# Optimization experiments

Hardware: AMD Instinct MI355X
Metric: run time of the kernel (lower is better)

## Reference

```python
import jax, jax.numpy as jnp
import numpy as np

Z_DIM = 3
H = 128
N_BLOCKS = 4
N = 30000
E = 180000
T = 2


def _mlp2(x, W1, b1, W2, b2):
    return jnp.maximum(x @ W1 + b1, 0.0) @ W2 + b2


def _stats(x, eps=1e-8):
    # batch mean/std as accumulated by the running-stat Normalizer (buffers -> no grad)
    m = x.mean(0)
    v = jnp.maximum((x * x).mean(0) - m * m, 0.0)
    s = jnp.maximum(jnp.sqrt(v), eps)
    return jax.lax.stop_gradient(m), jax.lax.stop_gradient(s)


def setup_inputs() -> dict:
    key = jax.random.key(0)
    ks = jax.random.split(key, 32)

    def w(k, shape, fan_in):
        return jax.random.normal(k, shape, jnp.float32) / np.sqrt(fan_in).astype(np.float32)

    inp = {}
    inp["z"] = jax.random.normal(ks[0], (T, N, Z_DIM), jnp.float32)
    inp["z_target"] = jax.random.normal(ks[1], (N, Z_DIM), jnp.float32)
    inp["pos"] = jax.random.uniform(ks[2], (N, 2), jnp.float32)
    # encoder node MLP: z_dim -> H -> H
    inp["enc_node_W1"] = w(ks[3], (Z_DIM, H), Z_DIM)
    inp["enc_node_b1"] = jnp.zeros((H,), jnp.float32)
    inp["enc_node_W2"] = w(ks[4], (H, H), H)
    inp["enc_node_b2"] = jnp.zeros((H,), jnp.float32)
    # encoder edge MLP: edge_dim(3) -> H -> H
    inp["enc_edge_W1"] = w(ks[5], (3, H), 3)
    inp["enc_edge_b1"] = jnp.zeros((H,), jnp.float32)
    inp["enc_edge_W2"] = w(ks[6], (H, H), H)
    inp["enc_edge_b2"] = jnp.zeros((H,), jnp.float32)
    # decoder MLP: H -> H -> z_dim
    inp["dec_W1"] = w(ks[7], (H, H), H)
    inp["dec_b1"] = jnp.zeros((H,), jnp.float32)
    inp["dec_W2"] = w(ks[8], (H, Z_DIM), H)
    inp["dec_b2"] = jnp.zeros((Z_DIM,), jnp.float32)
    # GraphNetBlocks, stacked over n_blocks
    inp["blk_edge_W1"] = w(ks[9], (N_BLOCKS, 3 * H, H), 3 * H)
    inp["blk_edge_b1"] = jnp.zeros((N_BLOCKS, H), jnp.float32)
    inp["blk_edge_W2"] = w(ks[10], (N_BLOCKS, H, H), H)
    inp["blk_edge_b2"] = jnp.zeros((N_BLOCKS, H), jnp.float32)
    inp["blk_node_W1"] = w(ks[11], (N_BLOCKS, 2 * H, H), 2 * H)
    inp["blk_node_b1"] = jnp.zeros((N_BLOCKS, H), jnp.float32)
    inp["blk_node_W2"] = w(ks[12], (N_BLOCKS, H, H), H)
    inp["blk_node_b2"] = jnp.zeros((N_BLOCKS, H), jnp.float32)
    # bidirectional mesh edges (triangles_to_edges output)
    inp["senders"] = jax.random.randint(ks[13], (E,), 0, N, jnp.int64)
    inp["receivers"] = jax.random.randint(ks[14], (E,), 0, N, jnp.int64)
    return inp


def reference(z, z_target, pos,
              enc_node_W1, enc_node_b1, enc_node_W2, enc_node_b2,
              enc_edge_W1, enc_edge_b1, enc_edge_W2, enc_edge_b2,
              dec_W1, dec_b1, dec_W2, dec_b2,
              blk_edge_W1, blk_edge_b1, blk_edge_W2, blk_edge_b2,
              blk_node_W1, blk_node_b1, blk_node_W2, blk_node_b2,
              senders, receivers):
    zl = z[-1]                                   # [N, z_dim]
    n_nodes = zl.shape[0]

    # --- build_graph ---
    rel = pos[senders] - pos[receivers]          # [E, 2]
    ef_raw = jnp.concatenate([rel, jnp.linalg.norm(rel, axis=1, keepdims=True)], axis=1)  # [E, 3]
    em, es = _stats(ef_raw)
    ef = _mlp2((ef_raw - em) / es, enc_edge_W1, enc_edge_b1, enc_edge_W2, enc_edge_b2)    # [E, H]
    nm, ns = _stats(zl)
    nf = _mlp2((zl - nm) / ns, enc_node_W1, enc_node_b1, enc_node_W2, enc_node_b2)        # [N, H]

    # --- message passing blocks ---
    def block(carry, p):
        nf, ef = carry
        eW1, eb1, eW2, eb2, nW1, nb1, nW2, nb2 = p
        e_in = jnp.concatenate([ef, nf[senders], nf[receivers]], axis=1)   # [E, 3H]
        ef = _mlp2(e_in, eW1, eb1, eW2, eb2) + ef
        agg = jax.ops.segment_sum(ef, receivers, num_segments=n_nodes)    # [N, H]
        n_in = jnp.concatenate([nf, agg], axis=1)                          # [N, 2H]
        nf = _mlp2(n_in, nW1, nb1, nW2, nb2) + nf
        return (nf, ef), None

    (nf, ef), _ = jax.lax.scan(block, (nf, ef),
                               (blk_edge_W1, blk_edge_b1, blk_edge_W2, blk_edge_b2,
                                blk_node_W1, blk_node_b1, blk_node_W2, blk_node_b2))

    # --- decode + loss ---
    output = _mlp2(nf, dec_W1, dec_b1, dec_W2, dec_b2)                     # [N, z_dim]
    target = z_target - zl
    om, os = _stats(target)
    target_normalized = (target - om) / os
    loss = jnp.mean((target_normalized - output) ** 2)

    z_update = jax.lax.stop_gradient(output) * os + om                     # Normalizer.inverse(detach)
    z_pred = zl + z_update
    rmse = jnp.mean(jnp.sqrt(jnp.mean((z_pred - z_target) ** 2, axis=0)))
    return z_pred, loss, rmse
```

## Files before the change

kernel.cpp:

```cpp
#include <hip/hip_runtime.h>
#include <hip/hip_bf16.h>
#include <math.h>

#define HDIM 128
#define TPB 256

typedef __attribute__((ext_vector_type(8))) short bf16x8;
typedef __attribute__((ext_vector_type(4))) float f32x4;

static inline int ceil_div(int a, int b){ return (a + b - 1) / b; }

__device__ __forceinline__ float wave_sum(float v){
#pragma unroll
  for (int o = 32; o > 0; o >>= 1) v += __shfl_down(v, o, 64);
  return v;
}

__device__ __forceinline__ short f2bf(float f){
  __hip_bfloat16 h = __float2bfloat16(f);
  return *reinterpret_cast<short*>(&h);
}
__device__ __forceinline__ float bfb2f(short s){
  unsigned int u = ((unsigned int)(unsigned short)s) << 16;
  return __builtin_bit_cast(float, u);
}

__device__ __forceinline__ void gl_lds16(const short* g, short* l){
  __builtin_amdgcn_global_load_lds(
      (const __attribute__((address_space(1))) void*)g,
      (__attribute__((address_space(3))) void*)l, 16, 0, 0);
}

__global__ void csr_hist(const int* __restrict__ rcv, int* __restrict__ deg, int E){
  int e = blockIdx.x * blockDim.x + threadIdx.x;
  if (e < E) atomicAdd(&deg[rcv[e]], 1);
}

__global__ void csr_scan(const int* __restrict__ deg, int* __restrict__ row_start,
                         int N, int E){
  __shared__ int part[1024];
  int t = threadIdx.x;
  int chunk = (N + 1023) / 1024;
  int lo = t * chunk, hi = min(lo + chunk, N);
  int s = 0;
  for (int i = lo; i < hi; i++) s += deg[i];
  part[t] = s;
  __syncthreads();
  for (int off = 1; off < 1024; off <<= 1){
    int v = (t >= off) ? part[t - off] : 0;
    __syncthreads();
    part[t] += v;
    __syncthreads();
  }
  int base = (t == 0) ? 0 : part[t - 1];
  for (int i = lo; i < hi; i++){
    row_start[i] = base;
    base += deg[i];
  }
  if (t == 1023) row_start[N] = E;
}

__global__ void edge_prep(const float* __restrict__ pos,
                          const int* __restrict__ snd,
                          const int* __restrict__ rcv,
                          int* __restrict__ cursor,
                          int* __restrict__ psnd,
                          int* __restrict__ prcv,
                          float* __restrict__ ef_raw,
                          float* __restrict__ epart, int E){
  __shared__ float red[4][6];
  int tid = threadIdx.x, w = tid >> 6, l = tid & 63;
  int e = blockIdx.x * blockDim.x + tid;
  float s[6] = {0.f,0.f,0.f,0.f,0.f,0.f};
  if (e < E){
    int si = snd[e], ri = rcv[e];
    int p = atomicAdd(&cursor[ri], 1);
    psnd[p] = si;
    prcv[p] = ri;
    float rx = pos[2*si]   - pos[2*ri];
    float ry = pos[2*si+1] - pos[2*ri+1];
    float nm = sqrtf(rx*rx + ry*ry);
    ef_raw[3*p]   = rx;
    ef_raw[3*p+1] = ry;
    ef_raw[3*p+2] = nm;
    s[0] = rx; s[1] = ry; s[2] = nm;
    s[3] = rx*rx; s[4] = ry*ry; s[5] = nm*nm;
  }
#pragma unroll
  for (int k = 0; k < 6; k++) s[k] = wave_sum(s[k]);
  if (l == 0)
#pragma unroll
    for (int k = 0; k < 6; k++) red[w][k] = s[k];
  __syncthreads();
  if (tid < 6)
    epart[(size_t)blockIdx.x * 6 + tid] =
      red[0][tid] + red[1][tid] + red[2][tid] + red[3][tid];
}

__global__ void node_stats(const float* __restrict__ zl,
                           const float* __restrict__ z_target,
                           float* __restrict__ npart, int N){
  __shared__ float red[4][12];
  int tid = threadIdx.x, w = tid >> 6, l = tid & 63;
  int n = blockIdx.x * blockDim.x + tid;
  float s[12];
#pragma unroll
  for (int i = 0; i < 12; i++) s[i] = 0.f;
  if (n < N){
#pragma unroll
    for (int d = 0; d < 3; d++){
      float z = zl[3*n+d];
      float t = z_target[3*n+d] - z;
      s[d]   = z;  s[3+d] = z*z;
      s[6+d] = t;  s[9+d] = t*t;
    }
  }
#pragma unroll
  for (int i = 0; i < 12; i++) s[i] = wave_sum(s[i]);
  if (l == 0)
#pragma unroll
    for (int i = 0; i < 12; i++) red[w][i] = s[i];
  __syncthreads();
  if (tid < 12)
    npart[(size_t)blockIdx.x * 12 + tid] =
      red[0][tid] + red[1][tid] + red[2][tid] + red[3][tid];
}

__global__ void reduce_stats(const float* __restrict__ ep, int ne,
                             const float* __restrict__ np_, int nn,
                             float* __restrict__ raw){
  __shared__ float red[4];
  int tid = threadIdx.x, w = tid >> 6, l = tid & 63;
  for (int j = 0; j < 6; j++){
    float s = 0.f;
    for (int b = tid; b < ne; b += 256) s += ep[(size_t)b * 6 + j];
    s = wave_sum(s);
    if (l == 0) red[w] = s;
    __syncthreads();
    if (tid == 0) raw[j] = red[0] + red[1] + red[2] + red[3];
    __syncthreads();
  }
  for (int j = 0; j < 12; j++){
    float s = 0.f;
    for (int b = tid; b < nn; b += 256) s += np_[(size_t)b * 12 + j];
    s = wave_sum(s);
    if (l == 0) red[w] = s;
    __syncthreads();
    if (tid == 0) raw[6 + j] = red[0] + red[1] + red[2] + red[3];
    __syncthreads();
  }
}

__global__ void finalize_stats(const float* __restrict__ raw,
                               float* __restrict__ fin, int E, int N){
#pragma unroll
  for (int d = 0; d < 3; d++){
    float cE = (float)E, cN = (float)N;
    float m, v;
    m = raw[0+d] / cE; v = fmaxf(raw[3+d]/cE - m*m, 0.f);
    fin[0+d] = m;  fin[3+d]  = fmaxf(sqrtf(v), 1e-8f);
    m = raw[6+d] / cN; v = fmaxf(raw[9+d]/cN - m*m, 0.f);
    fin[6+d] = m;  fin[9+d]  = fmaxf(sqrtf(v), 1e-8f);
    m = raw[12+d] / cN; v = fmaxf(raw[15+d]/cN - m*m, 0.f);
    fin[12+d] = m; fin[15+d] = fmaxf(sqrtf(v), 1e-8f);
  }
}

__global__ void pack_weights(const float* __restrict__ encEW2,
                             const float* __restrict__ encNW2,
                             const float* __restrict__ decW1,
                             const float* __restrict__ beW1,
                             const float* __restrict__ beW2,
                             const float* __restrict__ bnW1,
                             const float* __restrict__ bnW2,
                             __hip_bfloat16* __restrict__ wp){
  int y = blockIdx.y;
  const float* src; __hip_bfloat16* dst; int K;
  if (y == 0){ src = encEW2; dst = wp;          K = 128; }
  else if (y == 1){ src = encNW2; dst = wp + 16384; K = 128; }
  else if (y == 2){ src = decW1;  dst = wp + 32768; K = 128; }
  else {
    int b = (y - 3) >> 2, j = (y - 3) & 3;
    __hip_bfloat16* base = wp + 49152 + b * 114688;
    if (j == 0){ src = beW1 + b*49152; dst = base;          K = 384; }
    else if (j == 1){ src = beW2 + b*16384; dst = base + 49152; K = 128; }
    else if (j == 2){ src = bnW1 + b*32768; dst = base + 65536; K = 256; }
    else { src = bnW2 + b*16384; dst = base + 98304; K = 128; }
  }
  int id = blockIdx.x * blockDim.x + threadIdx.x;
  if (id >= 128 * K) return;
  int c = id >> 12;
  int r = id & 4095;
  int t = r >> 9;
  int l = (r >> 3) & 63;
  int j = r & 7;
  int k = c * 32 + ((l >> 4) << 3) + j;
  int n = t * 16 + (l & 15);
  dst[id] = __float2bfloat16(src[k * 128 + n]);
}

__launch_bounds__(256)
__global__ void encoder_fused(const float* __restrict__ raw,
                              const float* __restrict__ mptr,
                              const float* __restrict__ sptr,
                              const float* __restrict__ W1,
                              const float* __restrict__ b1,
                              const __hip_bfloat16* __restrict__ W2f,
                              const float* __restrict__ b2,
                              __hip_bfloat16* __restrict__ out, int rows){
  __shared__ __align__(16) short bsh[16384];
  const int tid = threadIdx.x, w = tid >> 6, l = tid & 63, m = l & 15, q = l >> 4;
  const short* wsrc = (const short*)W2f;
#pragma unroll
  for (int i = 0; i < 8; i++){
    int inst = w * 8 + i;
    gl_lds16(wsrc + inst * 512 + l * 8, &bsh[inst * 512]);
  }
  float s0 = mptr[0], s1 = mptr[1], s2 = mptr[2];
  float d0 = sptr[0], d1 = sptr[1], d2 = sptr[2];
  const int row0 = blockIdx.x * 64 + w * 16;
  const int ra = min(row0 + m, rows - 1);
  float x0 = (raw[3*ra]   - s0) / d0;
  float x1 = (raw[3*ra+1] - s1) / d1;
  float x2 = (raw[3*ra+2] - s2) / d2;
  bf16x8 afr[4];
#pragma unroll
  for (int c = 0; c < 4; c++){
    int nb = c * 32 + q * 8;
#pragma unroll
    for (int j = 0; j < 8; j++){
      float h = b1[nb+j] + x0 * W1[nb+j] + x1 * W1[128+nb+j] + x2 * W1[256+nb+j];
      afr[c][j] = f2bf(fmaxf(h, 0.f));
    }
  }
  f32x4 acc[8];
#pragma unroll
  for (int t = 0; t < 8; t++) acc[t] = (f32x4){0.f,0.f,0.f,0.f};
  __syncthreads();
#pragma unroll
  for (int c = 0; c < 4; c++){
#pragma unroll
    for (int t = 0; t < 8; t++){
      bf16x8 b = *(const bf16x8*)&bsh[(c*8 + t)*512 + l*8];
      acc[t] = __builtin_amdgcn_mfma_f32_16x16x32_bf16(afr[c], b, acc[t], 0, 0, 0);
    }
  }
  const int row_d = row0 + q * 4;
#pragma unroll
  for (int t = 0; t < 8; t++){
    int col = t * 16 + m;
    float bb = b2[col];
#pragma unroll
    for (int r = 0; r < 4; r++){
      int e = row_d + r;
      if (e < rows) out[(size_t)e * HDIM + col] = __float2bfloat16(acc[t][r] + bb);
    }
  }
}

__launch_bounds__(256)
__global__ void gemm128_g(const __hip_bfloat16* __restrict__ A,
                          const __hip_bfloat16* __restrict__ Wf,
                          const float* __restrict__ bias,
                          float* __restrict__ out, int rows){
  __shared__ __align__(16) short bsh[16384];
  const int tid = threadIdx.x, w = tid >> 6, l = tid & 63, m = l & 15, q = l >> 4;
  const short* wsrc = (const short*)Wf;
#pragma unroll
  for (int i = 0; i < 8; i++){
    int inst = w * 8 + i;
    gl_lds16(wsrc + inst * 512 + l * 8, &bsh[inst * 512]);
  }
  const int row0 = blockIdx.x * 64 + w * 16;
  const int ra = min(row0 + m, rows - 1);
  const short* pa = (const short*)A + (size_t)ra * HDIM + q * 8;
  bf16x8 afr[4];
#pragma unroll
  for (int c = 0; c < 4; c++) afr[c] = *(const bf16x8*)(pa + c * 32);
  f32x4 acc[8];
#pragma unroll
  for (int t = 0; t < 8; t++) acc[t] = (f32x4){0.f,0.f,0.f,0.f};
  __syncthreads();
#pragma unroll
  for (int c = 0; c < 4; c++){
#pragma unroll
    for (int t = 0; t < 8; t++){
      bf16x8 b = *(const bf16x8*)&bsh[(c*8 + t)*512 + l*8];
      acc[t] = __builtin_amdgcn_mfma_f32_16x16x32_bf16(afr[c], b, acc[t], 0, 0, 0);
    }
  }
  const int row_d = row0 + q * 4;
#pragma unroll
  for (int t = 0; t < 8; t++){
    int col = t * 16 + m;
    float bb = bias[col];
#pragma unroll
    for (int r = 0; r < 4; r++){
      int e = row_d + r;
      if (e < rows) out[(size_t)e * HDIM + col] = fmaxf(acc[t][r] + bb, 0.f);
    }
  }
}

__launch_bounds__(512)
__global__ void msg_pre(const __hip_bfloat16* __restrict__ nf,
                        const __hip_bfloat16* __restrict__ eWf,
                        __hip_bfloat16* __restrict__ u, int N){
  __shared__ __align__(16) short wsh[32768];
  const int tid = threadIdx.x, w = tid >> 6, l = tid & 63, m = l & 15, q = l >> 4;
  const short* wsrc = (const short*)eWf + 4 * 4096;
#pragma unroll
  for (int i = 0; i < 8; i++){
    int inst = w * 8 + i;
    gl_lds16(wsrc + inst * 512 + l * 8, &wsh[inst * 512]);
  }
  const int row0 = blockIdx.x * 128 + w * 16;
  const int ra = min(row0 + m, N - 1);
  const short* pa = (const short*)nf + (size_t)ra * HDIM + q * 8;
  bf16x8 afr[4];
#pragma unroll
  for (int c = 0; c < 4; c++) afr[c] = *(const bf16x8*)(pa + c * 32);
  f32x4 acc[16];
#pragma unroll
  for (int t = 0; t < 16; t++) acc[t] = (f32x4){0.f,0.f,0.f,0.f};
  __syncthreads();
#pragma unroll
  for (int c = 0; c < 4; c++){
#pragma unroll
    for (int t = 0; t < 16; t++){
      int cc = (t < 8) ? c : (4 + c);
      bf16x8 b = *(const bf16x8*)&wsh[cc * 4096 + (t & 7) * 512 + l * 8];
      acc[t] = __builtin_amdgcn_mfma_f32_16x16x32_bf16(afr[c], b, acc[t], 0, 0, 0);
    }
  }
  const int row_d = row0 + q * 4;
#pragma unroll
  for (int t = 0; t < 16; t++){
    int col = t * 16 + m;
#pragma unroll
    for (int r = 0; r < 4; r++){
      int n = row_d + r;
      if (n < N) u[(size_t)n * 256 + col] = __float2bfloat16(acc[t][r]);
    }
  }
}

__launch_bounds__(512)
__global__ void edge_block(const int* __restrict__ psnd,
                           const int* __restrict__ prcv,
                           const __hip_bfloat16* __restrict__ u,
                           __hip_bfloat16* __restrict__ ef,
                           const __hip_bfloat16* __restrict__ Wfrag,
                           const float* __restrict__ b1,
                           const float* __restrict__ b2,
                           int E){
  __shared__ __align__(16) short bsh[2][4096];
  __shared__ __align__(16) short hsh[8][16][136];
  const int tid = threadIdx.x, w = tid >> 6, l = tid & 63, m = l & 15, q = l >> 4;
  const short* wsrc = (const short*)Wfrag;
  gl_lds16(wsrc + w*512 + l*8, &bsh[0][w*512]);

  const int row0 = blockIdx.x * 128 + w * 16;
  const int ra = min(row0 + m, E - 1);
  const short* pe = (const short*)ef + (size_t)ra * HDIM + q * 8;
  bf16x8 afr[4];
#pragma unroll
  for (int c = 0; c < 4; c++) afr[c] = *(const bf16x8*)(pe + c * 32);

  {
    int grow = min(row0 + (l >> 2), E - 1);
    int us_row = psnd[grow], ur_row = prcv[grow];
    const short* pus = (const short*)u + (size_t)us_row * 256 + (l & 3) * 32;
    const short* pur = (const short*)u + (size_t)ur_row * 256 + 128 + (l & 3) * 32;
    short* hdst = &hsh[w][l >> 2][(l & 3) * 32];
#pragma unroll
    for (int k = 0; k < 4; k++){
      bf16x8 a = *(const bf16x8*)(pus + k * 8);
      bf16x8 b = *(const bf16x8*)(pur + k * 8);
      bf16x8 s;
#pragma unroll
      for (int j = 0; j < 8; j++) s[j] = f2bf(bfb2f(a[j]) + bfb2f(b[j]));
      *(bf16x8*)(hdst + k * 8) = s;
    }
  }
  const int orow = row0 + (l >> 2);
  const int orc = min(orow, E - 1);
  const short* pold = (const short*)ef + (size_t)orc * HDIM + (l & 3) * 32;
  bf16x8 vold[4];
#pragma unroll
  for (int k = 0; k < 4; k++) vold[k] = *(const bf16x8*)(pold + k * 8);

  f32x4 acc[8];
#pragma unroll
  for (int t = 0; t < 8; t++) acc[t] = (f32x4){0.f,0.f,0.f,0.f};
  __syncthreads();
#pragma unroll
  for (int c = 0; c < 4; c++){
    if (c + 1 < 4)
      gl_lds16(wsrc + (c+1)*4096 + w*512 + l*8, &bsh[(c+1)&1][w*512]);
    const short* bb = &bsh[c & 1][0];
#pragma unroll
    for (int t = 0; t < 8; t++){
      bf16x8 b = *(const bf16x8*)(bb + t*512 + l*8);
      acc[t] = __builtin_amdgcn_mfma_f32_16x16x32_bf16(afr[c], b, acc[t], 0, 0, 0);
    }
    if (c + 1 < 4) __syncthreads();
  }
#pragma unroll
  for (int t = 0; t < 8; t++){
    float bb = b1[t * 16 + m];
#pragma unroll
    for (int r = 0; r < 4; r++){
      float uval = bfb2f(hsh[w][q*4 + r][t*16 + m]);
      hsh[w][q*4 + r][t*16 + m] = f2bf(fmaxf(acc[t][r] + uval + bb, 0.f));
    }
  }
  const short* ph = &hsh[w][m][0] + q * 8;
  const short* w2 = wsrc + 49152;
  f32x4 acc2[8];
#pragma unroll
  for (int t = 0; t < 8; t++) acc2[t] = (f32x4){0.f,0.f,0.f,0.f};
#pragma unroll
  for (int c = 0; c < 4; c++){
    bf16x8 a = *(const bf16x8*)(ph + c * 32);
#pragma unroll
    for (int t = 0; t < 8; t++){
      bf16x8 b = *(const bf16x8*)(w2 + ((c*8 + t)*64 + l)*8);
      acc2[t] = __builtin_amdgcn_mfma_f32_16x16x32_bf16(a, b, acc2[t], 0, 0, 0);
    }
  }
#pragma unroll
  for (int t = 0; t < 8; t++){
    float bb = b2[t * 16 + m];
#pragma unroll
    for (int r = 0; r < 4; r++)
      hsh[w][q*4 + r][t*16 + m] = f2bf(acc2[t][r] + bb);
  }
  if (orow < E){
    const short* src = &hsh[w][l >> 2][(l & 3) * 32];
    short* dst = (short*)ef + (size_t)orow * HDIM + (l & 3) * 32;
#pragma unroll
    for (int k = 0; k < 4; k++){
      bf16x8 vnew = *(const bf16x8*)(src + k * 8);
      bf16x8 vo;
#pragma unroll
      for (int j = 0; j < 8; j++) vo[j] = f2bf(bfb2f(vnew[j]) + bfb2f(vold[k][j]));
      *(bf16x8*)(dst + k * 8) = vo;
    }
  }
}

__launch_bounds__(512)
__global__ void node_block(const int* __restrict__ row_start,
                           const __hip_bfloat16* __restrict__ ef,
                           __hip_bfloat16* __restrict__ nf,
                           const __hip_bfloat16* __restrict__ Wfrag,
                           const float* __restrict__ b1,
                           const float* __restrict__ b2,
                           int N){
  __shared__ __align__(16) short bsh[2][4096];
  __shared__ __align__(16) short hsh[8][16][136];
  const int tid = threadIdx.x, w = tid >> 6, l = tid & 63, m = l & 15, q = l >> 4;
  const short* wsrc = (const short*)Wfrag;
  gl_lds16(wsrc + w*512 + l*8, &bsh[0][w*512]);

  const int row0 = blockIdx.x * 128 + w * 16;
  const int ra = min(row0 + m, N - 1);
  const short* pn = (const short*)nf + (size_t)ra * HDIM + q * 8;
  bf16x8 afr[8];
#pragma unroll
  for (int c = 0; c < 4; c++) afr[c] = *(const bf16x8*)(pn + c * 32);
  const int orow = row0 + (l >> 2);
  const int orc = min(orow, N - 1);
  const short* pold = (const short*)nf + (size_t)orc * HDIM + (l & 3) * 32;
  bf16x8 vold[4];
#pragma unroll
  for (int k = 0; k < 4; k++) vold[k] = *(const bf16x8*)(pold + k * 8);

  float sum[4][8];
#pragma unroll
  for (int c = 0; c < 4; c++)
#pragma unroll
    for (int j = 0; j < 8; j++) sum[c][j] = 0.f;
  int s0 = row_start[ra], s1 = row_start[ra + 1];
  for (int it = s0; it < s1; it++){
    const short* pf = (const short*)ef + (size_t)it * HDIM + q * 8;
#pragma unroll
    for (int c = 0; c < 4; c++){
      bf16x8 v = *(const bf16x8*)(pf + c * 32);
#pragma unroll
      for (int j = 0; j < 8; j++) sum[c][j] += bfb2f(v[j]);
    }
  }
#pragma unroll
  for (int c = 0; c < 4; c++)
#pragma unroll
    for (int j = 0; j < 8; j++) afr[4 + c][j] = f2bf(sum[c][j]);

  f32x4 acc[8];
#pragma unroll
  for (int t = 0; t < 8; t++) acc[t] = (f32x4){0.f,0.f,0.f,0.f};
  __syncthreads();
#pragma unroll
  for (int c = 0; c < 8; c++){
    if (c + 1 < 8)
      gl_lds16(wsrc + (c+1)*4096 + w*512 + l*8, &bsh[(c+1)&1][w*512]);
    const short* bb = &bsh[c & 1][0];
#pragma unroll
    for (int t = 0; t < 8; t++){
      bf16x8 b = *(const bf16x8*)(bb + t*512 + l*8);
      acc[t] = __builtin_amdgcn_mfma_f32_16x16x32_bf16(afr[c], b, acc[t], 0, 0, 0);
    }
    if (c + 1 < 8) __syncthreads();
  }
#pragma unroll
  for (int t = 0; t < 8; t++){
    float bb = b1[t * 16 + m];
#pragma unroll
    for (int r = 0; r < 4; r++)
      hsh[w][q*4 + r][t*16 + m] = f2bf(fmaxf(acc[t][r] + bb, 0.f));
  }
  const short* ph = &hsh[w][m][0] + q * 8;
  const short* w2 = wsrc + 32768;
  f32x4 acc2[8];
#pragma unroll
  for (int t = 0; t < 8; t++) acc2[t] = (f32x4){0.f,0.f,0.f,0.f};
#pragma unroll
  for (int c = 0; c < 4; c++){
    bf16x8 a = *(const bf16x8*)(ph + c * 32);
#pragma unroll
    for (int t = 0; t < 8; t++){
      bf16x8 b = *(const bf16x8*)(w2 + ((c*8 + t)*64 + l)*8);
      acc2[t] = __builtin_amdgcn_mfma_f32_16x16x32_bf16(a, b, acc2[t], 0, 0, 0);
    }
  }
#pragma unroll
  for (int t = 0; t < 8; t++){
    float bb = b2[t * 16 + m];
#pragma unroll
    for (int r = 0; r < 4; r++)
      hsh[w][q*4 + r][t*16 + m] = f2bf(acc2[t][r] + bb);
  }
  if (orow < N){
    const short* src = &hsh[w][l >> 2][(l & 3) * 32];
    short* dst = (short*)nf + (size_t)orow * HDIM + (l & 3) * 32;
#pragma unroll
    for (int k = 0; k < 4; k++){
      bf16x8 vnew = *(const bf16x8*)(src + k * 8);
      bf16x8 vo;
#pragma unroll
      for (int j = 0; j < 8; j++) vo[j] = f2bf(bfb2f(vnew[j]) + bfb2f(vold[k][j]));
      *(bf16x8*)(dst + k * 8) = vo;
    }
  }
}

__global__ void dec_final(const float* __restrict__ hbuf,
                          const float* __restrict__ W2,
                          const float* __restrict__ b2,
                          float* __restrict__ outd, int rows){
  __shared__ float hl[64 * 129];
  __shared__ float Wl[HDIM * 3];
  __shared__ float bl[3];
  int t = threadIdx.x;
  int node0 = blockIdx.x * 64;
  for (int i = t; i < HDIM * 3; i += 256) Wl[i] = W2[i];
  if (t < 3) bl[t] = b2[t];
#pragma unroll
  for (int i = 0; i < 32; i++){
    int lin = t + i * 256;
    int r = lin >> 7;
    int c = lin & 127;
    int node = node0 + r;
    hl[r * 129 + c] = (node < rows) ? hbuf[(size_t)node * HDIM + c] : 0.f;
  }
  __syncthreads();
  if (t < 64){
    int node = node0 + t;
    if (node < rows){
      float a0 = bl[0], a1 = bl[1], a2 = bl[2];
      for (int k = 0; k < HDIM; k++){
        float v = hl[t * 129 + k];
        a0 += v * Wl[k * 3];
        a1 += v * Wl[k * 3 + 1];
        a2 += v * Wl[k * 3 + 2];
      }
      outd[3 * node]     = a0;
      outd[3 * node + 1] = a1;
      outd[3 * node + 2] = a2;
    }
  }
}

__global__ void epilogue(const float* __restrict__ dec_out,
                         const float* __restrict__ zl,
                         const float* __restrict__ z_target,
                         const float* __restrict__ fin,
                         float* __restrict__ d_out,
                         float* __restrict__ lpart, int N){
  __shared__ float red[4][4];
  int tid = threadIdx.x, w = tid >> 6, l = tid & 63;
  int n = blockIdx.x * blockDim.x + tid;
  float s[4] = {0.f,0.f,0.f,0.f};
  if (n < N){
#pragma unroll
    for (int d = 0; d < 3; d++){
      float om = fin[12 + d], os = fin[15 + d];
      float o   = dec_out[3*n + d];
      float zld = zl[3*n + d];
      float zt  = z_target[3*n + d];
      float tgt = zt - zld;
      float tn  = (tgt - om) / os;
      float diff = tn - o;
      s[0] += diff * diff;
      float zp = zld + o * os + om;
      d_out[3*n + d] = zp;
      float e = zp - zt;
      s[1 + d] = e * e;
    }
  }
#pragma unroll
  for (int k = 0; k < 4; k++) s[k] = wave_sum(s[k]);
  if (l == 0)
#pragma unroll
    for (int k = 0; k < 4; k++) red[w][k] = s[k];
  __syncthreads();
  if (tid < 4)
    lpart[(size_t)blockIdx.x * 4 + tid] =
      red[0][tid] + red[1][tid] + red[2][tid] + red[3][tid];
}

__global__ void finalize_out(const float* __restrict__ lpart, int nb,
                             float* __restrict__ d_out, int N){
  __shared__ float red[4];
  __shared__ float vals[4];
  int tid = threadIdx.x, w = tid >> 6, l = tid & 63;
  for (int j = 0; j < 4; j++){
    float s = 0.f;
    for (int b = tid; b < nb; b += 256) s += lpart[(size_t)b * 4 + j];
    s = wave_sum(s);
    if (l == 0) red[w] = s;
    __syncthreads();
    if (tid == 0) vals[j] = red[0] + red[1] + red[2] + red[3];
    __syncthreads();
  }
  if (tid == 0){
    float cN = (float)N;
    float loss = vals[0] / (3.f * cN);
    float rmse = (sqrtf(vals[1] / cN) + sqrtf(vals[2] / cN) + sqrtf(vals[3] / cN)) / 3.f;
    d_out[(size_t)3 * N]     = loss;
    d_out[(size_t)3 * N + 1] = rmse;
  }
}

extern "C" void kernel_launch(void* const* d_in, const int* in_sizes, int n_in,
                              void* d_out, int out_size, void* d_ws, size_t ws_size,
                              hipStream_t stream){
  const float* z           = (const float*)d_in[0];
  const float* z_target    = (const float*)d_in[1];
  const float* pos         = (const float*)d_in[2];
  const float* enc_node_W1 = (const float*)d_in[3];
  const float* enc_node_b1 = (const float*)d_in[4];
  const float* enc_node_W2 = (const float*)d_in[5];
  const float* enc_node_b2 = (const float*)d_in[6];
  const float* enc_edge_W1 = (const float*)d_in[7];
  const float* enc_edge_b1 = (const float*)d_in[8];
  const float* enc_edge_W2 = (const float*)d_in[9];
  const float* enc_edge_b2 = (const float*)d_in[10];
  const float* dec_W1      = (const float*)d_in[11];
  const float* dec_b1      = (const float*)d_in[12];
  const float* dec_W2      = (const float*)d_in[13];
  const float* dec_b2      = (const float*)d_in[14];
  const float* blk_edge_W1 = (const float*)d_in[15];
  const float* blk_edge_b1 = (const float*)d_in[16];
  const float* blk_edge_W2 = (const float*)d_in[17];
  const float* blk_edge_b2 = (const float*)d_in[18];
  const float* blk_node_W1 = (const float*)d_in[19];
  const float* blk_node_b1 = (const float*)d_in[20];
  const float* blk_node_W2 = (const float*)d_in[21];
  const float* blk_node_b2 = (const float*)d_in[22];
  const int*   senders     = (const int*)d_in[23];
  const int*   receivers   = (const int*)d_in[24];

  const int N = in_sizes[1] / 3;
  const int E = in_sizes[23];
  const float* zl = z + (size_t)N * 3;

  const int neb = ceil_div(E, TPB);
  const int nnb = ceil_div(N, TPB);

  char* p = (char*)d_ws;
  auto carve = [&](size_t bytes) -> char* {
    char* r = p; p += (bytes + 255) & ~(size_t)255; return r;
  };
  float* stats_raw = (float*)carve(32 * 4);
  float* stats_fin = (float*)carve(32 * 4);
  float* epart     = (float*)carve((size_t)neb * 6 * 4);
  float* npart     = (float*)carve((size_t)nnb * 12 * 4);
  float* lpart     = (float*)carve((size_t)nnb * 4 * 4);
  float* ef_raw    = (float*)carve((size_t)E * 3 * 4);
  float* dec_out   = (float*)carve((size_t)N * 3 * 4);
  float* hbuf      = (float*)carve((size_t)N * HDIM * 4);
  int*   deg       = (int*)carve((size_t)N * 4);
  int*   row_start = (int*)carve((size_t)(N + 1) * 4);
  int*   cursor    = (int*)carve((size_t)N * 4);
  int*   psnd      = (int*)carve((size_t)E * 4);
  int*   prcv      = (int*)carve((size_t)E * 4);
  __hip_bfloat16* wp = (__hip_bfloat16*)carve((size_t)507904 * 2);
  __hip_bfloat16* ef = (__hip_bfloat16*)carve((size_t)E * HDIM * 2);
  __hip_bfloat16* nf = (__hip_bfloat16*)carve((size_t)N * HDIM * 2);
  __hip_bfloat16* u  = (__hip_bfloat16*)carve((size_t)N * 256 * 2);

  float* out = (float*)d_out;

  hipMemsetAsync(deg, 0, (size_t)N * 4, stream);

  csr_hist<<<neb, TPB, 0, stream>>>(receivers, deg, E);
  csr_scan<<<1, 1024, 0, stream>>>(deg, row_start, N, E);
  hipMemcpyAsync(cursor, row_start, (size_t)N * 4, hipMemcpyDeviceToDevice, stream);
  edge_prep<<<neb, TPB, 0, stream>>>(pos, senders, receivers, cursor,
                                     psnd, prcv, ef_raw, epart, E);

  node_stats<<<nnb, TPB, 0, stream>>>(zl, z_target, npart, N);
  reduce_stats<<<1, TPB, 0, stream>>>(epart, neb, npart, nnb, stats_raw);
  finalize_stats<<<1, 1, 0, stream>>>(stats_raw, stats_fin, E, N);

  pack_weights<<<dim3(192, 19), TPB, 0, stream>>>(enc_edge_W2, enc_node_W2, dec_W1,
                                                  blk_edge_W1, blk_edge_W2,
                                                  blk_node_W1, blk_node_W2, wp);

  encoder_fused<<<ceil_div(E, 64), TPB, 0, stream>>>(ef_raw, stats_fin + 0, stats_fin + 3,
                                                     enc_edge_W1, enc_edge_b1,
                                                     wp, enc_edge_b2, ef, E);
  encoder_fused<<<ceil_div(N, 64), TPB, 0, stream>>>(zl, stats_fin + 6, stats_fin + 9,
                                                     enc_node_W1, enc_node_b1,
                                                     wp + 16384, enc_node_b2, nf, N);

  for (int b = 0; b < 4; b++){
    const __hip_bfloat16* eWf = wp + 49152 + (size_t)b * 114688;
    const __hip_bfloat16* nWf = eWf + 65536;
    const float* eb1 = blk_edge_b1 + (size_t)b * 128;
    const float* eb2 = blk_edge_b2 + (size_t)b * 128;
    const float* nb1 = blk_node_b1 + (size_t)b * 128;
    const float* nb2 = blk_node_b2 + (size_t)b * 128;

    msg_pre<<<ceil_div(N, 128), 512, 0, stream>>>(nf, eWf, u, N);
    edge_block<<<ceil_div(E, 128), 512, 0, stream>>>(psnd, prcv, u, ef,
                                                     eWf, eb1, eb2, E);
    node_block<<<ceil_div(N, 128), 512, 0, stream>>>(row_start, ef, nf,
                                                     nWf, nb1, nb2, N);
  }

  gemm128_g<<<ceil_div(N, 64), TPB, 0, stream>>>(nf, wp + 32768, dec_b1, hbuf, N);
  dec_final<<<ceil_div(N, 64), TPB, 0, stream>>>(hbuf, dec_W2, dec_b2, dec_out, N);

  epilogue<<<nnb, TPB, 0, stream>>>(dec_out, zl, z_target, stats_fin,
                                    out, lpart, N);
  finalize_out<<<1, TPB, 0, stream>>>(lpart, nnb, out, N);
}
```

Measured before the change: 556.9 us.

## Fuse next-block message precompute into node_block and merge small setup kernels

The per-block msg_pre launch for blocks after the first is folded into the tail of node_block. The freshly updated node features, already in LDS, are multiplied by the next block's sender/receiver weight slices and written to u, which avoids re-reading nf and one launch per block. The cursor copy is folded into csr_scan, and reduce_stats is merged with finalize_stats to drop launches. In exchange node_block does more work per launch and reads next-block weights straight from global memory rather than staging them, which may raise register pressure.

```diff
diff --git a/kernel.cpp b/kernel.cpp
--- a/kernel.cpp
+++ b/kernel.cpp
@@ -37,7 +37,7 @@
 }
 
 __global__ void csr_scan(const int* __restrict__ deg, int* __restrict__ row_start,
-                         int N, int E){
+                         int* __restrict__ cursor, int N, int E){
   __shared__ int part[1024];
   int t = threadIdx.x;
   int chunk = (N + 1023) / 1024;
@@ -55,6 +55,7 @@
   int base = (t == 0) ? 0 : part[t - 1];
   for (int i = lo; i < hi; i++){
     row_start[i] = base;
+    cursor[i]    = base;
     base += deg[i];
   }
   if (t == 1023) row_start[N] = E;
@@ -126,10 +127,11 @@
       red[0][tid] + red[1][tid] + red[2][tid] + red[3][tid];
 }
 
-__global__ void reduce_stats(const float* __restrict__ ep, int ne,
-                             const float* __restrict__ np_, int nn,
-                             float* __restrict__ raw){
+__global__ void reduce_finalize(const float* __restrict__ ep, int ne,
+                                const float* __restrict__ np_, int nn,
+                                float* __restrict__ fin, int E, int N){
   __shared__ float red[4];
+  __shared__ float raw[18];
   int tid = threadIdx.x, w = tid >> 6, l = tid & 63;
   for (int j = 0; j < 6; j++){
     float s = 0.f;
@@ -149,20 +151,18 @@
     if (tid == 0) raw[6 + j] = red[0] + red[1] + red[2] + red[3];
     __syncthreads();
   }
-}
-
-__global__ void finalize_stats(const float* __restrict__ raw,
-                               float* __restrict__ fin, int E, int N){
-#pragma unroll
-  for (int d = 0; d < 3; d++){
-    float cE = (float)E, cN = (float)N;
-    float m, v;
-    m = raw[0+d] / cE; v = fmaxf(raw[3+d]/cE - m*m, 0.f);
-    fin[0+d] = m;  fin[3+d]  = fmaxf(sqrtf(v), 1e-8f);
-    m = raw[6+d] / cN; v = fmaxf(raw[9+d]/cN - m*m, 0.f);
-    fin[6+d] = m;  fin[9+d]  = fmaxf(sqrtf(v), 1e-8f);
-    m = raw[12+d] / cN; v = fmaxf(raw[15+d]/cN - m*m, 0.f);
-    fin[12+d] = m; fin[15+d] = fmaxf(sqrtf(v), 1e-8f);
+  if (tid == 0){
+#pragma unroll
+    for (int d = 0; d < 3; d++){
+      float cE = (float)E, cN = (float)N;
+      float m, v;
+      m = raw[0+d] / cE; v = fmaxf(raw[3+d]/cE - m*m, 0.f);
+      fin[0+d] = m;  fin[3+d]  = fmaxf(sqrtf(v), 1e-8f);
+      m = raw[6+d] / cN; v = fmaxf(raw[9+d]/cN - m*m, 0.f);
+      fin[6+d] = m;  fin[9+d]  = fmaxf(sqrtf(v), 1e-8f);
+      m = raw[12+d] / cN; v = fmaxf(raw[15+d]/cN - m*m, 0.f);
+      fin[12+d] = m; fin[15+d] = fmaxf(sqrtf(v), 1e-8f);
+    }
   }
 }
 
@@ -457,6 +457,8 @@
                            const __hip_bfloat16* __restrict__ Wfrag,
                            const float* __restrict__ b1,
                            const float* __restrict__ b2,
+                           const __hip_bfloat16* __restrict__ eWf_next,
+                           __hip_bfloat16* __restrict__ u,
                            int N){
   __shared__ __align__(16) short bsh[2][4096];
   __shared__ __align__(16) short hsh[8][16][136];
@@ -541,16 +543,40 @@
     for (int r = 0; r < 4; r++)
       hsh[w][q*4 + r][t*16 + m] = f2bf(acc2[t][r] + bb);
   }
-  if (orow < N){
-    const short* src = &hsh[w][l >> 2][(l & 3) * 32];
+  {
+    short* srcm = &hsh[w][l >> 2][(l & 3) * 32];
     short* dst = (short*)nf + (size_t)orow * HDIM + (l & 3) * 32;
 #pragma unroll
     for (int k = 0; k < 4; k++){
-      bf16x8 vnew = *(const bf16x8*)(src + k * 8);
+      bf16x8 vnew = *(const bf16x8*)(srcm + k * 8);
       bf16x8 vo;
 #pragma unroll
       for (int j = 0; j < 8; j++) vo[j] = f2bf(bfb2f(vnew[j]) + bfb2f(vold[k][j]));
-      *(bf16x8*)(dst + k * 8) = vo;
+      if (orow < N) *(bf16x8*)(dst + k * 8) = vo;
+      *(bf16x8*)(srcm + k * 8) = vo;
+    }
+  }
+  if (eWf_next){
+    const short* wn = (const short*)eWf_next;
+    bf16x8 afr2[4];
+#pragma unroll
+    for (int c = 0; c < 4; c++) afr2[c] = *(const bf16x8*)(ph + c * 32);
+    const int row_d = row0 + q * 4;
+#pragma unroll
+    for (int t = 0; t < 16; t++){
+      f32x4 a3 = (f32x4){0.f,0.f,0.f,0.f};
+      const short* wbase = wn + ((t < 8) ? (4 + 0) : (8 + 0)) * 4096 + (t & 7) * 512 + l * 8;
+#pragma unroll
+      for (int c = 0; c < 4; c++){
+        bf16x8 b = *(const bf16x8*)(wbase + c * 4096);
+        a3 = __builtin_amdgcn_mfma_f32_16x16x32_bf16(afr2[c], b, a3, 0, 0, 0);
+      }
+      int col = t * 16 + m;
+#pragma unroll
+      for (int r = 0; r < 4; r++){
+        int n = row_d + r;
+        if (n < N) u[(size_t)n * 256 + col] = __float2bfloat16(a3[r]);
+      }
     }
   }
 }
@@ -693,7 +719,6 @@
   auto carve = [&](size_t bytes) -> char* {
     char* r = p; p += (bytes + 255) & ~(size_t)255; return r;
   };
-  float* stats_raw = (float*)carve(32 * 4);
   float* stats_fin = (float*)carve(32 * 4);
   float* epart     = (float*)carve((size_t)neb * 6 * 4);
   float* npart     = (float*)carve((size_t)nnb * 12 * 4);
@@ -716,14 +741,12 @@
   hipMemsetAsync(deg, 0, (size_t)N * 4, stream);
 
   csr_hist<<<neb, TPB, 0, stream>>>(receivers, deg, E);
-  csr_scan<<<1, 1024, 0, stream>>>(deg, row_start, N, E);
-  hipMemcpyAsync(cursor, row_start, (size_t)N * 4, hipMemcpyDeviceToDevice, stream);
+  csr_scan<<<1, 1024, 0, stream>>>(deg, row_start, cursor, N, E);
   edge_prep<<<neb, TPB, 0, stream>>>(pos, senders, receivers, cursor,
                                      psnd, prcv, ef_raw, epart, E);
 
   node_stats<<<nnb, TPB, 0, stream>>>(zl, z_target, npart, N);
-  reduce_stats<<<1, TPB, 0, stream>>>(epart, neb, npart, nnb, stats_raw);
-  finalize_stats<<<1, 1, 0, stream>>>(stats_raw, stats_fin, E, N);
+  reduce_finalize<<<1, TPB, 0, stream>>>(epart, neb, npart, nnb, stats_fin, E, N);
 
   pack_weights<<<dim3(192, 19), TPB, 0, stream>>>(enc_edge_W2, enc_node_W2, dec_W1,
                                                   blk_edge_W1, blk_edge_W2,
@@ -736,19 +759,22 @@
                                                      enc_node_W1, enc_node_b1,
                                                      wp + 16384, enc_node_b2, nf, N);
 
+  msg_pre<<<ceil_div(N, 128), 512, 0, stream>>>(nf, wp + 49152, u, N);
+
   for (int b = 0; b < 4; b++){
     const __hip_bfloat16* eWf = wp + 49152 + (size_t)b * 114688;
     const __hip_bfloat16* nWf = eWf + 65536;
+    const __hip_bfloat16* eWf_next = (b < 3) ? (eWf + 114688) : nullptr;
     const float* eb1 = blk_edge_b1 + (size_t)b * 128;
     const float* eb2 = blk_edge_b2 + (size_t)b * 128;
     const float* nb1 = blk_node_b1 + (size_t)b * 128;
     const float* nb2 = blk_node_b2 + (size_t)b * 128;
 
-    msg_pre<<<ceil_div(N, 128), 512, 0, stream>>>(nf, eWf, u, N);
     edge_block<<<ceil_div(E, 128), 512, 0, stream>>>(psnd, prcv, u, ef,
                                                      eWf, eb1, eb2, E);
     node_block<<<ceil_div(N, 128), 512, 0, stream>>>(row_start, ef, nf,
-                                                     nWf, nb1, nb2, N);
+                                                     nWf, nb1, nb2,
+                                                     eWf_next, u, N);
   }
 
   gemm128_g<<<ceil_div(N, 64), TPB, 0, stream>>>(nf, wp + 32768, dec_b1, hbuf, N);
```

Measured after the change: 583.6 us. +4.8%, slower.
